# Kernel tuning notes

Hardware: AMD Instinct MI355X
Metric: run time of the kernel (lower is better)

The kernel has to match this reference:

```python
import jax, jax.numpy as jnp
import numpy as np

VOCAB = 32000
EMB = 256
HID = 512
BATCH = 32
MAXLEN = 64
START_TOKEN = 0


def setup_inputs() -> dict:
    key = jax.random.key(0)
    ks = jax.random.split(key, 10)
    return {
        "encoder_outputs": jax.random.normal(ks[0], (BATCH, 64, HID), dtype=jnp.float32),
        "encoder_hidden": jax.random.normal(ks[1], (1, BATCH, HID), dtype=jnp.float32),
        "target_tensor": jax.random.randint(ks[2], (BATCH, MAXLEN), 0, VOCAB),
        "embedding": jax.random.normal(ks[3], (VOCAB, EMB), dtype=jnp.float32) * 0.02,
        "W_ih": jax.random.normal(ks[4], (3 * HID, EMB), dtype=jnp.float32) * 0.05,
        "W_hh": jax.random.normal(ks[5], (3 * HID, HID), dtype=jnp.float32) * 0.05,
        "b_ih": jax.random.normal(ks[6], (3 * HID,), dtype=jnp.float32) * 0.05,
        "b_hh": jax.random.normal(ks[7], (3 * HID,), dtype=jnp.float32) * 0.05,
        "W_out": jax.random.normal(ks[8], (VOCAB, HID), dtype=jnp.float32) * 0.05,
        "b_out": jax.random.normal(ks[9], (VOCAB,), dtype=jnp.float32) * 0.05,
    }


def _gru_scan(x_seq, h0, W_ih, W_hh, b_ih, b_hh):
    # x_seq: [T, B, E]; h0: [B, H]. torch nn.GRU gate math/order (r, z, n).
    def step(h, x):
        gi = x @ W_ih.T + b_ih            # [B, 3H]
        gh = h @ W_hh.T + b_hh            # [B, 3H]
        i_r, i_z, i_n = jnp.split(gi, 3, axis=-1)
        h_r, h_z, h_n = jnp.split(gh, 3, axis=-1)
        r = jax.nn.sigmoid(i_r + h_r)
        z = jax.nn.sigmoid(i_z + h_z)
        n = jnp.tanh(i_n + r * h_n)
        h_new = (1.0 - z) * n + z * h
        return h_new, h_new
    hT, ys = jax.lax.scan(step, h0, x_seq)
    return ys, hT


def reference(encoder_outputs, encoder_hidden, target_tensor, embedding,
              W_ih, W_hh, b_ih, b_hh, W_out, b_out):
    B = encoder_outputs.shape[0]
    # Teacher forcing: step 0 consumes START, step i consumes target[:, i-1].
    start = jnp.full((B, 1), START_TOKEN, dtype=target_tensor.dtype)
    dec_in = jnp.concatenate([start, target_tensor[:, :-1]], axis=1)  # [B, T]
    # embed -> (dropout p=0 is identity) -> relu
    emb = jax.nn.relu(embedding[dec_in])                # [B, T, E]
    x_seq = jnp.swapaxes(emb, 0, 1)                     # [T, B, E]
    h0 = encoder_hidden[0]                              # [B, H] (num_layers=1)
    ys, hT = _gru_scan(x_seq, h0, W_ih, W_hh, b_ih, b_hh)  # ys: [T, B, H]
    hidden_seq = jnp.swapaxes(ys, 0, 1)                 # [B, T, H]
    logits = jnp.einsum("bth,vh->btv", hidden_seq, W_out) + b_out  # [B, T, V]
    log_probs = jax.nn.log_softmax(logits, axis=-1)
    decoder_hidden = hT[None]                           # [1, B, H]
    return log_probs, decoder_hidden
```

## Files before the change

kernel.cpp:

```cpp
#include <hip/hip_runtime.h>
#include <hip/hip_bf16.h>
#include <math.h>


typedef __bf16 bf16x8 __attribute__((ext_vector_type(8)));
typedef float  f32x4  __attribute__((ext_vector_type(4)));
typedef unsigned short u16;
typedef u16 u16x8v __attribute__((ext_vector_type(8)));
typedef u16 u16x4v __attribute__((ext_vector_type(4)));

#define BTV (32L * 64 * 32000)
#define LDC2 64000L

#define OFF_X    (0L)
#define SZ_X     (2048L * 256 * 2)
#define OFF_WIH  (OFF_X + SZ_X)
#define SZ_WIH   (1536L * 256 * 2)
#define OFF_WHH  (OFF_WIH + SZ_WIH)
#define SZ_WHH   (1536L * 512 * 2)
#define OFF_WOUT (OFF_WHH + SZ_WHH)
#define SZ_WOUT  (32000L * 512 * 2)
#define OFF_GI   (OFF_WOUT + SZ_WOUT)
#define SZ_GI    (2048L * 1536 * 4)
#define OFF_HS   (OFF_GI + SZ_GI)
#define SZ_HS    (2048L * 512 * 2)
#define OFF_FLG  (OFF_HS + SZ_HS)
#define SZ_FLG   (512L)
#define OFF_EV   (OFF_FLG + SZ_FLG)
#define SZ_EV    (64L)
#define WS_NEED  (OFF_EV + SZ_EV)

__device__ __forceinline__ u16 f2bf(float f) {
  union { float f; unsigned u; } a; a.f = f;
  unsigned r = a.u + 0x7fffu + ((a.u >> 16) & 1u);
  return (u16)(r >> 16);
}

__device__ __forceinline__ float bf2f(u16 u) {
  union { unsigned u; float f; } a; a.u = ((unsigned)u) << 16;
  return a.f;
}

__device__ __forceinline__ void gload16(const void* g, void* l) {
  __builtin_amdgcn_global_load_lds(
      (const __attribute__((address_space(1))) unsigned int*)g,
      (__attribute__((address_space(3))) unsigned int*)l, 16, 0, 0);
}

extern "C" __global__ void k_cast(const float* __restrict__ s, u16* __restrict__ d, int n4) {
  int i = blockIdx.x * blockDim.x + threadIdx.x;
  int st = gridDim.x * blockDim.x;
  for (; i < n4; i += st) {
    float4 v = reinterpret_cast<const float4*>(s)[i];
    u16x4v o; o.x = f2bf(v.x); o.y = f2bf(v.y); o.z = f2bf(v.z); o.w = f2bf(v.w);
    reinterpret_cast<u16x4v*>(d)[i] = o;
  }
}

extern "C" __global__ void k_embed(const float* __restrict__ emb, const int* __restrict__ tgt,
                                   u16* __restrict__ X) {
  int idx = blockIdx.x * 256 + threadIdx.x;
  int row = idx >> 5;
  int c8  = (idx & 31) << 3;
  int t = row >> 5, b = row & 31;
  int token = (t == 0) ? 0 : tgt[b * 64 + t - 1];
  const float* e = emb + (long)token * 256 + c8;
  u16x8v o;
#pragma unroll
  for (int i = 0; i < 8; ++i) { float v = e[i]; o[i] = f2bf(v > 0.f ? v : 0.f); }
  *reinterpret_cast<u16x8v*>(X + (long)row * 256 + c8) = o;
}

extern "C" __global__ void k_init(unsigned* flags, unsigned* evars) {
  int i = threadIdx.x;
  if (i < 128) {
    unsigned z = 0u;
    asm volatile("global_store_dword %0, %1, off sc0 sc1"
                 :: "v"(flags + i), "v"(z) : "memory");
  }
  if (i < 10) atomicExch(&evars[i], i == 8 ? 0xFFFFFFFFu : 0u);
}

template <bool BF16OUT>
__global__ void __launch_bounds__(256)
k_gemm_t(const u16* __restrict__ A, const u16* __restrict__ B,
         const float* __restrict__ bias, float* __restrict__ C,
         u16* __restrict__ C2, int M, int N, int K, long ldc2) {
  __shared__ u16 At[128 * 32];
  __shared__ u16 Bt[128 * 32];
  int mt = M >> 7;
  int bn = blockIdx.x / mt, bm = blockIdx.x % mt;
  int tid = threadIdx.x, wave = tid >> 6, lane = tid & 63;
  int wr = wave >> 1, wc = wave & 1;
  f32x4 acc[4][4] = {};
  const u16* ga = A + (long)(bm * 128 + wave * 32 + (lane >> 2)) * K + ((lane & 3) << 3);
  const u16* gb = B + (long)(bn * 128 + wave * 32 + (lane >> 2)) * K + ((lane & 3) << 3);
  u16* la0 = &At[wave * 1024]; u16* la1 = la0 + 512;
  u16* lb0 = &Bt[wave * 1024]; u16* lb1 = lb0 + 512;
  long k16 = 16L * K;
  for (int k0 = 0; k0 < K; k0 += 32) {
    if (k0) __syncthreads();
    gload16(ga + k0, la0);
    gload16(ga + k16 + k0, la1);
    gload16(gb + k0, lb0);
    gload16(gb + k16 + k0, lb1);
    __syncthreads();
    bf16x8 af[4], bfr[4];
#pragma unroll
    for (int mi = 0; mi < 4; ++mi)
      af[mi] = *reinterpret_cast<const bf16x8*>(
          &At[(wr * 64 + mi * 16 + (lane & 15)) * 32 + ((lane >> 4) << 3)]);
#pragma unroll
    for (int ni = 0; ni < 4; ++ni)
      bfr[ni] = *reinterpret_cast<const bf16x8*>(
          &Bt[(wc * 64 + ni * 16 + (lane & 15)) * 32 + ((lane >> 4) << 3)]);
#pragma unroll
    for (int mi = 0; mi < 4; ++mi)
#pragma unroll
      for (int ni = 0; ni < 4; ++ni)
        acc[mi][ni] = __builtin_amdgcn_mfma_f32_16x16x32_bf16(af[mi], bfr[ni], acc[mi][ni], 0, 0, 0);
  }
  int rb = bm * 128 + wr * 64 + ((lane >> 4) << 2);
  int cb = bn * 128 + wc * 64 + (lane & 15);
#pragma unroll
  for (int mi = 0; mi < 4; ++mi)
#pragma unroll
    for (int ni = 0; ni < 4; ++ni) {
      int col = cb + ni * 16;
      float bv = bias[col];
#pragma unroll
      for (int q = 0; q < 4; ++q) {
        int rr = rb + mi * 16 + q;
        if (BF16OUT) C2[(long)rr * ldc2 + col] = f2bf(acc[mi][ni][q] + bv);
        else         C[(long)rr * N + col] = acc[mi][ni][q] + bv;
      }
    }
}

extern "C" __global__ void __launch_bounds__(768, 1)
k_gru6(const float* __restrict__ gi, const u16* __restrict__ Whh,
       const float* __restrict__ bhh, const float* __restrict__ eh,
       u16* __restrict__ HS, float* __restrict__ outH,
       unsigned* flags, unsigned* evars) {
  __shared__ u16 Ah[32 * 512];
  __shared__ float gh[3][2][32][66];
  __shared__ int role_s;
  int tid = threadIdx.x, wave = tid >> 6, lane = tid & 63;
  if (tid == 0) {
    unsigned xcc;
    asm volatile("s_getreg_b32 %0, hwreg(20, 0, 32)" : "=s"(xcc));
    xcc &= 7u;
    unsigned arr = atomicAdd(&evars[xcc], 1u);
    if (arr == 7u) atomicCAS(&evars[8], 0xFFFFFFFFu, xcc);
    unsigned L = 0xFFFFFFFFu;
    for (int it = 0; it < (1 << 24) && L == 0xFFFFFFFFu; ++it) {
      asm volatile("global_load_dword %0, %1, off sc0 sc1\n\ts_waitcnt vmcnt(0)"
                   : "=v"(L) : "v"(evars + 8) : "memory");
    }
    int role = -1;
    if (L == xcc) {
      unsigned c = atomicAdd(&evars[9], 1u);
      if (c < 8u) role = (int)c;
    }
    role_s = role;
  }
  __syncthreads();
  int g = role_s;
  if (g < 0) return;
  int j0 = g * 64;
  int gate = wave >> 2, uh = (wave >> 1) & 1, sig = wave & 1;
  bf16x8 barr[2][8];
  {
    const u16* wbase = Whh + (long)(gate * 512 + j0 + uh * 32) * 512 + sig * 256;
#pragma unroll
    for (int ut = 0; ut < 2; ++ut)
#pragma unroll
      for (int kt = 0; kt < 8; ++kt)
        barr[ut][kt] = *reinterpret_cast<const bf16x8*>(
            wbase + (long)(ut * 16 + (lane & 15)) * 512 + kt * 32 + ((lane >> 4) << 3));
  }
  bool act2 = tid < 512;
  float hprev[3] = {}, bb0[3] = {}, bb1[3] = {}, bb2[3] = {};
  const float* gp0; const float* gp1; const float* gp2 = nullptr;
  u16* hs0; u16* hs1; u16* hs2 = nullptr;
  int b_[3], u_[3];
#pragma unroll
  for (int s = 0; s < 3; ++s) {
    int o = s * 768 + tid;
    if (o < 2048) {
      int b = o >> 6, u = o & 63, j = j0 + u;
      b_[s] = b; u_[s] = u;
      hprev[s] = eh[b * 512 + j];
      bb0[s] = bhh[j]; bb1[s] = bhh[512 + j]; bb2[s] = bhh[1024 + j];
    } else { b_[s] = 0; u_[s] = 0; }
  }
  gp0 = gi + b_[0] * 1536 + j0 + u_[0];
  gp1 = gi + b_[1] * 1536 + j0 + u_[1];
  if (act2) gp2 = gi + b_[2] * 1536 + j0 + u_[2];
  hs0 = HS + ((long)b_[0] * 64) * 512 + j0 + u_[0];
  hs1 = HS + ((long)b_[1] * 64) * 512 + j0 + u_[1];
  if (act2) hs2 = HS + ((long)b_[2] * 64) * 512 + j0 + u_[2];
  const char* sp0 = nullptr; const char* sp1 = nullptr;
  const char* sp2 = nullptr; const char* sp3 = nullptr;
  char* ld0 = nullptr; char* ld1 = nullptr; char* ld2 = nullptr; char* ld3 = nullptr;
  if (tid < 512) {
#pragma unroll
    for (int l = 0; l < 4; ++l) {
      int n = l * 512 + tid;
      int row = n >> 6, i = n & 63;
      const char* sp = (const char*)HS + (long)row * 65536 + i * 16 - 1024;
      char* ld = (char*)Ah + row * 1024 + ((i * 16) ^ ((row & 7) << 4));
      if (l == 0) { sp0 = sp; ld0 = ld; } else if (l == 1) { sp1 = sp; ld1 = ld; }
      else if (l == 2) { sp2 = sp; ld2 = ld; } else { sp3 = sp; ld3 = ld; }
    }
#pragma unroll
    for (int l = 0; l < 4; ++l) {
      int n = l * 512 + tid;
      int row = n >> 6, i = n & 63;
      const float* p = eh + row * 512 + i * 8;
      float4 aa = *reinterpret_cast<const float4*>(p);
      float4 bb = *reinterpret_cast<const float4*>(p + 4);
      u16x8v o8;
      o8[0] = f2bf(aa.x); o8[1] = f2bf(aa.y); o8[2] = f2bf(aa.z); o8[3] = f2bf(aa.w);
      o8[4] = f2bf(bb.x); o8[5] = f2bf(bb.y); o8[6] = f2bf(bb.z); o8[7] = f2bf(bb.w);
      *reinterpret_cast<u16x8v*>((char*)Ah + row * 1024 + ((i * 16) ^ ((row & 7) << 4))) = o8;
    }
  }
  const float K1 = -1.44269504f, K2 = 2.88539009f;
  for (int t = 0; t < 64; ++t) {
    float gr0 = gp0[0], gz0 = gp0[512], gn0 = gp0[1024];
    float gr1 = gp1[0], gz1 = gp1[512], gn1 = gp1[1024];
    float gr2 = 0.f, gz2 = 0.f, gn2 = 0.f;
    if (act2) { gr2 = gp2[0]; gz2 = gp2[512]; gn2 = gp2[1024]; }
    gp0 += 49152; gp1 += 49152; if (act2) gp2 += 49152;
    if (t) {
      if (wave == 0) {
        const unsigned* fp = flags + (lane & 7) * 16;
        unsigned v;
        do {
          asm volatile("global_load_dword %0, %1, off sc0 sc1\n\ts_waitcnt vmcnt(0)"
                       : "=v"(v) : "v"(fp) : "memory");
        } while (!__all((int)(v >= (unsigned)t)));
      }
      __syncthreads();
      if (tid < 512) {
        f32x4 d0, d1, d2, d3;
        asm volatile(
            "global_load_dwordx4 %0, %4, off sc0\n\t"
            "global_load_dwordx4 %1, %5, off sc0\n\t"
            "global_load_dwordx4 %2, %6, off sc0\n\t"
            "global_load_dwordx4 %3, %7, off sc0\n\t"
            "s_waitcnt vmcnt(0)"
            : "=v"(d0), "=v"(d1), "=v"(d2), "=v"(d3)
            : "v"(sp0), "v"(sp1), "v"(sp2), "v"(sp3)
            : "memory");
        *reinterpret_cast<f32x4*>(ld0) = d0;
        *reinterpret_cast<f32x4*>(ld1) = d1;
        *reinterpret_cast<f32x4*>(ld2) = d2;
        *reinterpret_cast<f32x4*>(ld3) = d3;
      }
    }
    if (tid < 512) { sp0 += 1024; sp1 += 1024; sp2 += 1024; sp3 += 1024; }
    __syncthreads();
    f32x4 acc[2][2] = {};
    int r15 = lane & 15;
    int cbyte = sig * 512 + ((lane >> 4) << 4);
#pragma unroll
    for (int kt = 0; kt < 8; ++kt) {
      bf16x8 a0 = *reinterpret_cast<const bf16x8*>(
          (const char*)Ah + r15 * 1024 + ((kt * 64 + cbyte) ^ ((r15 & 7) << 4)));
      bf16x8 a1 = *reinterpret_cast<const bf16x8*>(
          (const char*)Ah + (16 + r15) * 1024 + ((kt * 64 + cbyte) ^ ((r15 & 7) << 4)));
#pragma unroll
      for (int ut = 0; ut < 2; ++ut) {
        acc[0][ut] = __builtin_amdgcn_mfma_f32_16x16x32_bf16(a0, barr[ut][kt], acc[0][ut], 0, 0, 0);
        acc[1][ut] = __builtin_amdgcn_mfma_f32_16x16x32_bf16(a1, barr[ut][kt], acc[1][ut], 0, 0, 0);
      }
    }
    {
      int ucol = uh * 32 + r15;
      int brow = (lane >> 4) << 2;
#pragma unroll
      for (int q = 0; q < 4; ++q) {
        gh[gate][sig][brow + q][ucol]           = acc[0][0][q];
        gh[gate][sig][brow + q][ucol + 16]      = acc[0][1][q];
        gh[gate][sig][16 + brow + q][ucol]      = acc[1][0][q];
        gh[gate][sig][16 + brow + q][ucol + 16] = acc[1][1][q];
      }
    }
    __syncthreads();
#pragma unroll
    for (int s = 0; s < 3; ++s) {
      if (s == 2 && !act2) break;
      int b = b_[s], u = u_[s];
      float gr = s == 0 ? gr0 : s == 1 ? gr1 : gr2;
      float gz = s == 0 ? gz0 : s == 1 ? gz1 : gz2;
      float gn = s == 0 ? gn0 : s == 1 ? gn1 : gn2;
      float hr = gh[0][0][b][u] + gh[0][1][b][u] + bb0[s];
      float hz = gh[1][0][b][u] + gh[1][1][b][u] + bb1[s];
      float hn = gh[2][0][b][u] + gh[2][1][b][u] + bb2[s];
      float r = 1.f / (1.f + __builtin_amdgcn_exp2f(K1 * (gr + hr)));
      float z = 1.f / (1.f + __builtin_amdgcn_exp2f(K1 * (gz + hz)));
      float x = gn + r * hn;
      float th = 1.f - 2.f / (1.f + __builtin_amdgcn_exp2f(K2 * x));
      float hnew = th + z * (hprev[s] - th);
      hprev[s] = hnew;
      unsigned hb = (unsigned)f2bf(hnew);
      u16* hp = s == 0 ? hs0 : s == 1 ? hs1 : hs2;
      asm volatile("global_store_short %0, %1, off sc0"
                   :: "v"(hp), "v"(hb) : "memory");
    }
    hs0 += 512; hs1 += 512; if (act2) hs2 += 512;
    asm volatile("s_waitcnt vmcnt(0)" ::: "memory");
    __syncthreads();
    if (tid == 0) {
      unsigned ph = (unsigned)(t + 1);
      asm volatile("global_store_dword %0, %1, off sc0 sc1\n\ts_waitcnt vmcnt(0)"
                   :: "v"(flags + g * 16), "v"(ph) : "memory");
    }
  }
#pragma unroll
  for (int s = 0; s < 3; ++s) {
    if (s == 2 && !act2) break;
    outH[b_[s] * 512 + j0 + u_[s]] = hprev[s];
  }
}

extern "C" __global__ void __launch_bounds__(512)
k_lsm_b(const u16* __restrict__ LGbase, float* __restrict__ P) {
  extern __shared__ u16 srb[];
  __shared__ float red[8];
  const u16* LG = LGbase + (long)blockIdx.x * LDC2;
  float* out = P + (long)blockIdx.x * 32000;
  int tid = threadIdx.x, wave = tid >> 6, lane = tid & 63;
  float mx = -INFINITY;
  for (int i = tid; i < 4000; i += 512) {
    u16x8v v = reinterpret_cast<const u16x8v*>(LG)[i];
    reinterpret_cast<u16x8v*>(srb)[i] = v;
#pragma unroll
    for (int e = 0; e < 8; ++e) mx = fmaxf(mx, bf2f(v[e]));
  }
#pragma unroll
  for (int off = 32; off; off >>= 1) mx = fmaxf(mx, __shfl_down(mx, off, 64));
  if (lane == 0) red[wave] = mx;
  __syncthreads();
  if (tid == 0) {
    float m = red[0];
#pragma unroll
    for (int w = 1; w < 8; ++w) m = fmaxf(m, red[w]);
    red[0] = m;
  }
  __syncthreads();
  mx = red[0];
  __syncthreads();
  float sm = 0.f;
  for (int i = tid; i < 4000; i += 512) {
    u16x8v v = reinterpret_cast<const u16x8v*>(srb)[i];
#pragma unroll
    for (int e = 0; e < 8; ++e) sm += __expf(bf2f(v[e]) - mx);
  }
#pragma unroll
  for (int off = 32; off; off >>= 1) sm += __shfl_down(sm, off, 64);
  if (lane == 0) red[wave] = sm;
  __syncthreads();
  if (tid == 0) {
    float s = 0.f;
#pragma unroll
    for (int w = 0; w < 8; ++w) s += red[w];
    red[0] = mx + __logf(s);
  }
  __syncthreads();
  float L = red[0];
  for (int i = tid; i < 4000; i += 512) {
    u16x8v v = reinterpret_cast<const u16x8v*>(srb)[i];
    float4 o1, o2;
    o1.x = bf2f(v[0]) - L; o1.y = bf2f(v[1]) - L; o1.z = bf2f(v[2]) - L; o1.w = bf2f(v[3]) - L;
    o2.x = bf2f(v[4]) - L; o2.y = bf2f(v[5]) - L; o2.z = bf2f(v[6]) - L; o2.w = bf2f(v[7]) - L;
    reinterpret_cast<float4*>(out + (long)i * 8)[0] = o1;
    reinterpret_cast<float4*>(out + (long)i * 8)[1] = o2;
  }
}

extern "C" void kernel_launch(void* const* d_in, const int* in_sizes, int n_in,
                              void* d_out, int out_size, void* d_ws, size_t ws_size,
                              hipStream_t stream) {
  (void)in_sizes; (void)n_in; (void)out_size;
  const float* enc_hid = (const float*)d_in[1];
  const int*   tgt     = (const int*)d_in[2];
  const float* emb     = (const float*)d_in[3];
  const float* W_ih    = (const float*)d_in[4];
  const float* W_hh    = (const float*)d_in[5];
  const float* b_ih    = (const float*)d_in[6];
  const float* b_hh    = (const float*)d_in[7];
  const float* W_out   = (const float*)d_in[8];
  const float* b_out   = (const float*)d_in[9];
  float* out = (float*)d_out;
  char* ws = (char*)d_ws;
  if (ws_size < (size_t)WS_NEED) return;

  u16* X        = (u16*)(ws + OFF_X);
  u16* Wih      = (u16*)(ws + OFF_WIH);
  u16* Whh      = (u16*)(ws + OFF_WHH);
  u16* Wout     = (u16*)(ws + OFF_WOUT);
  float* gi     = (float*)(ws + OFF_GI);
  u16* HS       = (u16*)(ws + OFF_HS);
  unsigned* flg = (unsigned*)(ws + OFF_FLG);
  unsigned* ev  = (unsigned*)(ws + OFF_EV);
  u16* LG       = (u16*)d_out;

  hipFuncSetAttribute(reinterpret_cast<const void*>(k_lsm_b),
                      hipFuncAttributeMaxDynamicSharedMemorySize, 65536);

  k_cast<<<96, 256, 0, stream>>>(W_ih, Wih, 1536 * 256 / 4);
  k_cast<<<192, 256, 0, stream>>>(W_hh, Whh, 1536 * 512 / 4);
  k_cast<<<2048, 256, 0, stream>>>(W_out, Wout, 32000 * 512 / 4);
  k_embed<<<256, 256, 0, stream>>>(emb, tgt, X);
  k_init<<<1, 256, 0, stream>>>(flg, ev);
  k_gemm_t<false><<<(1536 / 128) * (2048 / 128), 256, 0, stream>>>(
      X, Wih, b_ih, gi, nullptr, 2048, 1536, 256, 0);
  k_gru6<<<64, 768, 0, stream>>>(gi, Whh, b_hh, enc_hid, HS, out + BTV, flg, ev);
  k_gemm_t<true><<<(32000 / 128) * (2048 / 128), 256, 0, stream>>>(
      HS, Wout, b_out, nullptr, LG, 2048, 32000, 512, LDC2);
  k_lsm_b<<<2048, 512, 64000, stream>>>(LG, out);
}
```

Measured before the change: 450.3 us.

## Fuse GRU recurrence and output projection into one persistent megakernel

The GRU recurrence and the vocabulary projection GEMM are merged into a single persistent kernel. Eight blocks run the GRU, and the remaining blocks poll per-step flags to start projection tiles for time steps whose hidden states are complete, so the large GEMM overlaps the serial recurrence. HS is re-laid out time-major so that each row tile corresponds to finished time steps, with output rows remapped back. Both GEMMs gain double-buffered LDS prefetch. The risks are spin-wait overhead, three blocks sharing a CU with the latency-critical GRU blocks, and possible deadlock if the co-residency assumptions do not hold.

Measured after the change: 734.9 us. 63.2% more time.

```diff
diff --git a/kernel.cpp b/kernel.cpp
--- a/kernel.cpp
+++ b/kernel.cpp
@@ -11,6 +11,8 @@
 
 #define BTV (32L * 64 * 32000)
 #define LDC2 64000L
+#define NPROJ 248
+#define NTILES 4000
 
 #define OFF_X    (0L)
 #define SZ_X     (2048L * 256 * 2)
@@ -25,7 +27,7 @@
 #define OFF_HS   (OFF_GI + SZ_GI)
 #define SZ_HS    (2048L * 512 * 2)
 #define OFF_FLG  (OFF_HS + SZ_HS)
-#define SZ_FLG   (512L)
+#define SZ_FLG   (1024L)
 #define OFF_EV   (OFF_FLG + SZ_FLG)
 #define SZ_EV    (64L)
 #define WS_NEED  (OFF_EV + SZ_EV)
@@ -73,21 +75,20 @@
 
 extern "C" __global__ void k_init(unsigned* flags, unsigned* evars) {
   int i = threadIdx.x;
-  if (i < 128) {
+  if (i < 256) {
     unsigned z = 0u;
     asm volatile("global_store_dword %0, %1, off sc0 sc1"
                  :: "v"(flags + i), "v"(z) : "memory");
   }
-  if (i < 10) atomicExch(&evars[i], i == 8 ? 0xFFFFFFFFu : 0u);
-}
-
-template <bool BF16OUT>
-__global__ void __launch_bounds__(256)
-k_gemm_t(const u16* __restrict__ A, const u16* __restrict__ B,
-         const float* __restrict__ bias, float* __restrict__ C,
-         u16* __restrict__ C2, int M, int N, int K, long ldc2) {
-  __shared__ u16 At[128 * 32];
-  __shared__ u16 Bt[128 * 32];
+  if (i < 12) atomicExch(&evars[i], i == 8 ? 0xFFFFFFFFu : 0u);
+}
+
+extern "C" __global__ void __launch_bounds__(256)
+k_gemm_gi(const u16* __restrict__ A, const u16* __restrict__ B,
+          const float* __restrict__ bias, float* __restrict__ C,
+          int M, int N, int K) {
+  __shared__ u16 At[2][4096];
+  __shared__ u16 Bt[2][4096];
   int mt = M >> 7;
   int bn = blockIdx.x / mt, bm = blockIdx.x % mt;
   int tid = threadIdx.x, wave = tid >> 6, lane = tid & 63;
@@ -95,30 +96,39 @@
   f32x4 acc[4][4] = {};
   const u16* ga = A + (long)(bm * 128 + wave * 32 + (lane >> 2)) * K + ((lane & 3) << 3);
   const u16* gb = B + (long)(bn * 128 + wave * 32 + (lane >> 2)) * K + ((lane & 3) << 3);
-  u16* la0 = &At[wave * 1024]; u16* la1 = la0 + 512;
-  u16* lb0 = &Bt[wave * 1024]; u16* lb1 = lb0 + 512;
   long k16 = 16L * K;
+  {
+    u16* la0 = &At[0][wave * 1024]; u16* lb0 = &Bt[0][wave * 1024];
+    gload16(ga, la0); gload16(ga + k16, la0 + 512);
+    gload16(gb, lb0); gload16(gb + k16, lb0 + 512);
+  }
+  asm volatile("s_waitcnt vmcnt(0)" ::: "memory");
+  __syncthreads();
+  int cur = 0;
   for (int k0 = 0; k0 < K; k0 += 32) {
-    if (k0) __syncthreads();
-    gload16(ga + k0, la0);
-    gload16(ga + k16 + k0, la1);
-    gload16(gb + k0, lb0);
-    gload16(gb + k16 + k0, lb1);
-    __syncthreads();
+    if (k0 + 32 < K) {
+      int nb = cur ^ 1;
+      u16* la0 = &At[nb][wave * 1024]; u16* lb0 = &Bt[nb][wave * 1024];
+      gload16(ga + k0 + 32, la0); gload16(ga + k16 + k0 + 32, la0 + 512);
+      gload16(gb + k0 + 32, lb0); gload16(gb + k16 + k0 + 32, lb0 + 512);
+    }
     bf16x8 af[4], bfr[4];
 #pragma unroll
     for (int mi = 0; mi < 4; ++mi)
       af[mi] = *reinterpret_cast<const bf16x8*>(
-          &At[(wr * 64 + mi * 16 + (lane & 15)) * 32 + ((lane >> 4) << 3)]);
+          &At[cur][(wr * 64 + mi * 16 + (lane & 15)) * 32 + ((lane >> 4) << 3)]);
 #pragma unroll
     for (int ni = 0; ni < 4; ++ni)
       bfr[ni] = *reinterpret_cast<const bf16x8*>(
-          &Bt[(wc * 64 + ni * 16 + (lane & 15)) * 32 + ((lane >> 4) << 3)]);
+          &Bt[cur][(wc * 64 + ni * 16 + (lane & 15)) * 32 + ((lane >> 4) << 3)]);
 #pragma unroll
     for (int mi = 0; mi < 4; ++mi)
 #pragma unroll
       for (int ni = 0; ni < 4; ++ni)
         acc[mi][ni] = __builtin_amdgcn_mfma_f32_16x16x32_bf16(af[mi], bfr[ni], acc[mi][ni], 0, 0, 0);
+    asm volatile("s_waitcnt vmcnt(0)" ::: "memory");
+    __syncthreads();
+    cur ^= 1;
   }
   int rb = bm * 128 + wr * 64 + ((lane >> 4) << 2);
   int cb = bn * 128 + wc * 64 + (lane & 15);
@@ -131,20 +141,21 @@
 #pragma unroll
       for (int q = 0; q < 4; ++q) {
         int rr = rb + mi * 16 + q;
-        if (BF16OUT) C2[(long)rr * ldc2 + col] = f2bf(acc[mi][ni][q] + bv);
-        else         C[(long)rr * N + col] = acc[mi][ni][q] + bv;
-      }
-    }
-}
-
-extern "C" __global__ void __launch_bounds__(768, 1)
-k_gru6(const float* __restrict__ gi, const u16* __restrict__ Whh,
+        C[(long)rr * N + col] = acc[mi][ni][q] + bv;
+      }
+    }
+}
+
+extern "C" __global__ void __launch_bounds__(768, 3)
+k_mega(const float* __restrict__ gi, const u16* __restrict__ Whh,
        const float* __restrict__ bhh, const float* __restrict__ eh,
        u16* __restrict__ HS, float* __restrict__ outH,
-       unsigned* flags, unsigned* evars) {
-  __shared__ u16 Ah[32 * 512];
-  __shared__ float gh[3][2][32][66];
+       unsigned* flags, unsigned* evars,
+       const u16* __restrict__ Wout, const float* __restrict__ bout,
+       u16* __restrict__ LG) {
+  extern __shared__ char arena[];
   __shared__ int role_s;
+  __shared__ int pidx_s;
   int tid = threadIdx.x, wave = tid >> 6, lane = tid & 63;
   if (tid == 0) {
     unsigned xcc;
@@ -166,163 +177,251 @@
   }
   __syncthreads();
   int g = role_s;
-  if (g < 0) return;
-  int j0 = g * 64;
-  int gate = wave >> 2, uh = (wave >> 1) & 1, sig = wave & 1;
-  bf16x8 barr[2][8];
-  {
-    const u16* wbase = Whh + (long)(gate * 512 + j0 + uh * 32) * 512 + sig * 256;
-#pragma unroll
-    for (int ut = 0; ut < 2; ++ut)
-#pragma unroll
-      for (int kt = 0; kt < 8; ++kt)
-        barr[ut][kt] = *reinterpret_cast<const bf16x8*>(
-            wbase + (long)(ut * 16 + (lane & 15)) * 512 + kt * 32 + ((lane >> 4) << 3));
-  }
-  bool act2 = tid < 512;
-  float hprev[3] = {}, bb0[3] = {}, bb1[3] = {}, bb2[3] = {};
-  const float* gp0; const float* gp1; const float* gp2 = nullptr;
-  u16* hs0; u16* hs1; u16* hs2 = nullptr;
-  int b_[3], u_[3];
-#pragma unroll
-  for (int s = 0; s < 3; ++s) {
-    int o = s * 768 + tid;
-    if (o < 2048) {
-      int b = o >> 6, u = o & 63, j = j0 + u;
-      b_[s] = b; u_[s] = u;
-      hprev[s] = eh[b * 512 + j];
-      bb0[s] = bhh[j]; bb1[s] = bhh[512 + j]; bb2[s] = bhh[1024 + j];
-    } else { b_[s] = 0; u_[s] = 0; }
-  }
-  gp0 = gi + b_[0] * 1536 + j0 + u_[0];
-  gp1 = gi + b_[1] * 1536 + j0 + u_[1];
-  if (act2) gp2 = gi + b_[2] * 1536 + j0 + u_[2];
-  hs0 = HS + ((long)b_[0] * 64) * 512 + j0 + u_[0];
-  hs1 = HS + ((long)b_[1] * 64) * 512 + j0 + u_[1];
-  if (act2) hs2 = HS + ((long)b_[2] * 64) * 512 + j0 + u_[2];
-  const char* sp0 = nullptr; const char* sp1 = nullptr;
-  const char* sp2 = nullptr; const char* sp3 = nullptr;
-  char* ld0 = nullptr; char* ld1 = nullptr; char* ld2 = nullptr; char* ld3 = nullptr;
-  if (tid < 512) {
-#pragma unroll
-    for (int l = 0; l < 4; ++l) {
-      int n = l * 512 + tid;
-      int row = n >> 6, i = n & 63;
-      const char* sp = (const char*)HS + (long)row * 65536 + i * 16 - 1024;
-      char* ld = (char*)Ah + row * 1024 + ((i * 16) ^ ((row & 7) << 4));
-      if (l == 0) { sp0 = sp; ld0 = ld; } else if (l == 1) { sp1 = sp; ld1 = ld; }
-      else if (l == 2) { sp2 = sp; ld2 = ld; } else { sp3 = sp; ld3 = ld; }
-    }
-#pragma unroll
-    for (int l = 0; l < 4; ++l) {
-      int n = l * 512 + tid;
-      int row = n >> 6, i = n & 63;
-      const float* p = eh + row * 512 + i * 8;
-      float4 aa = *reinterpret_cast<const float4*>(p);
-      float4 bb = *reinterpret_cast<const float4*>(p + 4);
-      u16x8v o8;
-      o8[0] = f2bf(aa.x); o8[1] = f2bf(aa.y); o8[2] = f2bf(aa.z); o8[3] = f2bf(aa.w);
-      o8[4] = f2bf(bb.x); o8[5] = f2bf(bb.y); o8[6] = f2bf(bb.z); o8[7] = f2bf(bb.w);
-      *reinterpret_cast<u16x8v*>((char*)Ah + row * 1024 + ((i * 16) ^ ((row & 7) << 4))) = o8;
-    }
-  }
-  const float K1 = -1.44269504f, K2 = 2.88539009f;
-  for (int t = 0; t < 64; ++t) {
-    float gr0 = gp0[0], gz0 = gp0[512], gn0 = gp0[1024];
-    float gr1 = gp1[0], gz1 = gp1[512], gn1 = gp1[1024];
-    float gr2 = 0.f, gz2 = 0.f, gn2 = 0.f;
-    if (act2) { gr2 = gp2[0]; gz2 = gp2[512]; gn2 = gp2[1024]; }
-    gp0 += 49152; gp1 += 49152; if (act2) gp2 += 49152;
-    if (t) {
-      if (wave == 0) {
-        const unsigned* fp = flags + (lane & 7) * 16;
-        unsigned v;
-        do {
-          asm volatile("global_load_dword %0, %1, off sc0 sc1\n\ts_waitcnt vmcnt(0)"
-                       : "=v"(v) : "v"(fp) : "memory");
-        } while (!__all((int)(v >= (unsigned)t)));
-      }
-      __syncthreads();
-      if (tid < 512) {
-        f32x4 d0, d1, d2, d3;
-        asm volatile(
-            "global_load_dwordx4 %0, %4, off sc0\n\t"
-            "global_load_dwordx4 %1, %5, off sc0\n\t"
-            "global_load_dwordx4 %2, %6, off sc0\n\t"
-            "global_load_dwordx4 %3, %7, off sc0\n\t"
-            "s_waitcnt vmcnt(0)"
-            : "=v"(d0), "=v"(d1), "=v"(d2), "=v"(d3)
-            : "v"(sp0), "v"(sp1), "v"(sp2), "v"(sp3)
-            : "memory");
-        *reinterpret_cast<f32x4*>(ld0) = d0;
-        *reinterpret_cast<f32x4*>(ld1) = d1;
-        *reinterpret_cast<f32x4*>(ld2) = d2;
-        *reinterpret_cast<f32x4*>(ld3) = d3;
-      }
-    }
-    if (tid < 512) { sp0 += 1024; sp1 += 1024; sp2 += 1024; sp3 += 1024; }
-    __syncthreads();
-    f32x4 acc[2][2] = {};
+
+  if (g >= 0) {
+    u16* Ah = (u16*)arena;
+    float (*gh)[2][32][66] = (float (*)[2][32][66])(arena + 32768);
+    int j0 = g * 64;
+    int gate = wave >> 2, uh = (wave >> 1) & 1, sig = wave & 1;
+    bf16x8 barr[2][8];
+    {
+      const u16* wbase = Whh + (long)(gate * 512 + j0 + uh * 32) * 512 + sig * 256;
+#pragma unroll
+      for (int ut = 0; ut < 2; ++ut)
+#pragma unroll
+        for (int kt = 0; kt < 8; ++kt)
+          barr[ut][kt] = *reinterpret_cast<const bf16x8*>(
+              wbase + (long)(ut * 16 + (lane & 15)) * 512 + kt * 32 + ((lane >> 4) << 3));
+    }
+    bool act2 = tid < 512;
+    float hprev[3] = {}, bb0[3] = {}, bb1[3] = {}, bb2[3] = {};
+    int b_[3], u_[3];
+#pragma unroll
+    for (int s = 0; s < 3; ++s) {
+      int o = s * 768 + tid;
+      if (o < 2048) {
+        int b = o >> 6, u = o & 63, j = j0 + u;
+        b_[s] = b; u_[s] = u;
+        hprev[s] = eh[b * 512 + j];
+        bb0[s] = bhh[j]; bb1[s] = bhh[512 + j]; bb2[s] = bhh[1024 + j];
+      } else { b_[s] = 0; u_[s] = 0; }
+    }
+    const float* gp0 = gi + (long)b_[0] * 1536 + j0 + u_[0];
+    const float* gp1 = gi + (long)b_[1] * 1536 + j0 + u_[1];
+    const float* gp2 = act2 ? gi + (long)b_[2] * 1536 + j0 + u_[2] : nullptr;
+    u16* hs0 = HS + (long)b_[0] * 512 + j0 + u_[0];
+    u16* hs1 = HS + (long)b_[1] * 512 + j0 + u_[1];
+    u16* hs2 = act2 ? HS + (long)b_[2] * 512 + j0 + u_[2] : nullptr;
+    const char* sp0 = nullptr; const char* sp1 = nullptr;
+    const char* sp2 = nullptr; const char* sp3 = nullptr;
+    char* ld0 = nullptr; char* ld1 = nullptr; char* ld2 = nullptr; char* ld3 = nullptr;
+    if (tid < 512) {
+#pragma unroll
+      for (int l = 0; l < 4; ++l) {
+        int n = l * 512 + tid;
+        int row = n >> 6, i = n & 63;
+        char* ld = (char*)Ah + row * 1024 + ((i * 16) ^ ((row & 7) << 4));
+        const char* sp = (const char*)HS + (long)n * 16 - 32768;
+        if (l == 0) { sp0 = sp; ld0 = ld; } else if (l == 1) { sp1 = sp; ld1 = ld; }
+        else if (l == 2) { sp2 = sp; ld2 = ld; } else { sp3 = sp; ld3 = ld; }
+      }
+#pragma unroll
+      for (int l = 0; l < 4; ++l) {
+        int n = l * 512 + tid;
+        int row = n >> 6, i = n & 63;
+        const float* p = eh + row * 512 + i * 8;
+        float4 aa = *reinterpret_cast<const float4*>(p);
+        float4 bb = *reinterpret_cast<const float4*>(p + 4);
+        u16x8v o8;
+        o8[0] = f2bf(aa.x); o8[1] = f2bf(aa.y); o8[2] = f2bf(aa.z); o8[3] = f2bf(aa.w);
+        o8[4] = f2bf(bb.x); o8[5] = f2bf(bb.y); o8[6] = f2bf(bb.z); o8[7] = f2bf(bb.w);
+        *reinterpret_cast<u16x8v*>((char*)Ah + row * 1024 + ((i * 16) ^ ((row & 7) << 4))) = o8;
+      }
+    }
     int r15 = lane & 15;
     int cbyte = sig * 512 + ((lane >> 4) << 4);
-#pragma unroll
-    for (int kt = 0; kt < 8; ++kt) {
-      bf16x8 a0 = *reinterpret_cast<const bf16x8*>(
-          (const char*)Ah + r15 * 1024 + ((kt * 64 + cbyte) ^ ((r15 & 7) << 4)));
-      bf16x8 a1 = *reinterpret_cast<const bf16x8*>(
-          (const char*)Ah + (16 + r15) * 1024 + ((kt * 64 + cbyte) ^ ((r15 & 7) << 4)));
-#pragma unroll
-      for (int ut = 0; ut < 2; ++ut) {
-        acc[0][ut] = __builtin_amdgcn_mfma_f32_16x16x32_bf16(a0, barr[ut][kt], acc[0][ut], 0, 0, 0);
-        acc[1][ut] = __builtin_amdgcn_mfma_f32_16x16x32_bf16(a1, barr[ut][kt], acc[1][ut], 0, 0, 0);
-      }
-    }
-    {
-      int ucol = uh * 32 + r15;
-      int brow = (lane >> 4) << 2;
-#pragma unroll
-      for (int q = 0; q < 4; ++q) {
-        gh[gate][sig][brow + q][ucol]           = acc[0][0][q];
-        gh[gate][sig][brow + q][ucol + 16]      = acc[0][1][q];
-        gh[gate][sig][16 + brow + q][ucol]      = acc[1][0][q];
-        gh[gate][sig][16 + brow + q][ucol + 16] = acc[1][1][q];
-      }
-    }
-    __syncthreads();
+    int ucol = uh * 32 + r15;
+    int brow = (lane >> 4) << 2;
+    const float K1 = -1.44269504f, K2 = 2.88539009f;
+    for (int t = 0; t < 64; ++t) {
+      float gr0 = gp0[0], gz0 = gp0[512], gn0 = gp0[1024]; gp0 += 49152;
+      float gr1 = gp1[0], gz1 = gp1[512], gn1 = gp1[1024]; gp1 += 49152;
+      float gr2 = 0.f, gz2 = 0.f, gn2 = 0.f;
+      if (act2) { gr2 = gp2[0]; gz2 = gp2[512]; gn2 = gp2[1024]; gp2 += 49152; }
+      if (t) {
+        if (wave == 0) {
+          const unsigned* fp = flags + (lane & 7) * 16;
+          unsigned v;
+          do {
+            asm volatile("global_load_dword %0, %1, off sc0 sc1\n\ts_waitcnt vmcnt(0)"
+                         : "=v"(v) : "v"(fp) : "memory");
+          } while (!__all((int)(v >= (unsigned)t)));
+        }
+        __syncthreads();
+        if (tid < 512) {
+          f32x4 d0, d1, d2, d3;
+          asm volatile(
+              "global_load_dwordx4 %0, %4, off sc0\n\t"
+              "global_load_dwordx4 %1, %5, off sc0\n\t"
+              "global_load_dwordx4 %2, %6, off sc0\n\t"
+              "global_load_dwordx4 %3, %7, off sc0\n\t"
+              "s_waitcnt vmcnt(0)"
+              : "=v"(d0), "=v"(d1), "=v"(d2), "=v"(d3)
+              : "v"(sp0), "v"(sp1), "v"(sp2), "v"(sp3)
+              : "memory");
+          *reinterpret_cast<f32x4*>(ld0) = d0;
+          *reinterpret_cast<f32x4*>(ld1) = d1;
+          *reinterpret_cast<f32x4*>(ld2) = d2;
+          *reinterpret_cast<f32x4*>(ld3) = d3;
+        }
+      }
+      if (tid < 512) { sp0 += 32768; sp1 += 32768; sp2 += 32768; sp3 += 32768; }
+      __syncthreads();
+      {
+        f32x4 acc[2][2] = {};
+#pragma unroll
+        for (int kt = 0; kt < 8; ++kt) {
+          bf16x8 a0 = *reinterpret_cast<const bf16x8*>(
+              (const char*)Ah + r15 * 1024 + ((kt * 64 + cbyte) ^ ((r15 & 7) << 4)));
+          bf16x8 a1 = *reinterpret_cast<const bf16x8*>(
+              (const char*)Ah + (16 + r15) * 1024 + ((kt * 64 + cbyte) ^ ((r15 & 7) << 4)));
+#pragma unroll
+          for (int ut = 0; ut < 2; ++ut) {
+            acc[0][ut] = __builtin_amdgcn_mfma_f32_16x16x32_bf16(a0, barr[ut][kt], acc[0][ut], 0, 0, 0);
+            acc[1][ut] = __builtin_amdgcn_mfma_f32_16x16x32_bf16(a1, barr[ut][kt], acc[1][ut], 0, 0, 0);
+          }
+        }
+#pragma unroll
+        for (int q = 0; q < 4; ++q) {
+          gh[gate][sig][brow + q][ucol]           = acc[0][0][q];
+          gh[gate][sig][brow + q][ucol + 16]      = acc[0][1][q];
+          gh[gate][sig][16 + brow + q][ucol]      = acc[1][0][q];
+          gh[gate][sig][16 + brow + q][ucol + 16] = acc[1][1][q];
+        }
+      }
+      __syncthreads();
+#pragma unroll
+      for (int s = 0; s < 3; ++s) {
+        if (s == 2 && !act2) break;
+        int b = b_[s], u = u_[s];
+        float gr = s == 0 ? gr0 : s == 1 ? gr1 : gr2;
+        float gz = s == 0 ? gz0 : s == 1 ? gz1 : gz2;
+        float gn = s == 0 ? gn0 : s == 1 ? gn1 : gn2;
+        float hr = gh[0][0][b][u] + gh[0][1][b][u] + bb0[s];
+        float hz = gh[1][0][b][u] + gh[1][1][b][u] + bb1[s];
+        float hn = gh[2][0][b][u] + gh[2][1][b][u] + bb2[s];
+        float r = 1.f / (1.f + __builtin_amdgcn_exp2f(K1 * (gr + hr)));
+        float z = 1.f / (1.f + __builtin_amdgcn_exp2f(K1 * (gz + hz)));
+        float x = gn + r * hn;
+        float th = 1.f - 2.f / (1.f + __builtin_amdgcn_exp2f(K2 * x));
+        float hnew = th + z * (hprev[s] - th);
+        hprev[s] = hnew;
+        unsigned hb = (unsigned)f2bf(hnew);
+        u16* hp = s == 0 ? hs0 : s == 1 ? hs1 : hs2;
+        asm volatile("global_store_short %0, %1, off sc0 sc1"
+                     :: "v"(hp), "v"(hb) : "memory");
+      }
+      hs0 += 16384; hs1 += 16384; if (act2) hs2 += 16384;
+      asm volatile("s_waitcnt vmcnt(0)" ::: "memory");
+      __syncthreads();
+      if (tid == 704) {
+        unsigned ph = (unsigned)(t + 1);
+        asm volatile("global_store_dword %0, %1, off sc0 sc1\n\ts_waitcnt vmcnt(0)"
+                     :: "v"(flags + g * 16), "v"(ph) : "memory");
+      }
+    }
 #pragma unroll
     for (int s = 0; s < 3; ++s) {
       if (s == 2 && !act2) break;
-      int b = b_[s], u = u_[s];
-      float gr = s == 0 ? gr0 : s == 1 ? gr1 : gr2;
-      float gz = s == 0 ? gz0 : s == 1 ? gz1 : gz2;
-      float gn = s == 0 ? gn0 : s == 1 ? gn1 : gn2;
-      float hr = gh[0][0][b][u] + gh[0][1][b][u] + bb0[s];
-      float hz = gh[1][0][b][u] + gh[1][1][b][u] + bb1[s];
-      float hn = gh[2][0][b][u] + gh[2][1][b][u] + bb2[s];
-      float r = 1.f / (1.f + __builtin_amdgcn_exp2f(K1 * (gr + hr)));
-      float z = 1.f / (1.f + __builtin_amdgcn_exp2f(K1 * (gz + hz)));
-      float x = gn + r * hn;
-      float th = 1.f - 2.f / (1.f + __builtin_amdgcn_exp2f(K2 * x));
-      float hnew = th + z * (hprev[s] - th);
-      hprev[s] = hnew;
-      unsigned hb = (unsigned)f2bf(hnew);
-      u16* hp = s == 0 ? hs0 : s == 1 ? hs1 : hs2;
-      asm volatile("global_store_short %0, %1, off sc0"
-                   :: "v"(hp), "v"(hb) : "memory");
-    }
-    hs0 += 512; hs1 += 512; if (act2) hs2 += 512;
+      outH[b_[s] * 512 + j0 + u_[s]] = hprev[s];
+    }
+    return;
+  }
+
+  if (tid == 0) pidx_s = (int)atomicAdd(&evars[10], 1u);
+  __syncthreads();
+  int p = pidx_s;
+  int grp = wave >> 2, wv = wave & 3;
+  int wr = wv >> 1, wc = wv & 1;
+  u16* At = (u16*)(arena + grp * 32768);
+  u16* Bt = At + 8192;
+  const long k16 = 16L * 512;
+  for (long round = 0;; ++round) {
+    long base = 3L * p + 3L * NPROJ * round;
+    if (base >= NTILES) break;
+    int lastTile = (int)((base + 2 < NTILES) ? base + 2 : (NTILES - 1));
+    unsigned need = 4u * (unsigned)(lastTile / 250) + 4u;
+    if (wave == 0) {
+      const unsigned* fp = flags + (lane & 7) * 16;
+      unsigned v; int it = 0;
+      for (;;) {
+        asm volatile("global_load_dword %0, %1, off sc0 sc1\n\ts_waitcnt vmcnt(0)"
+                     : "=v"(v) : "v"(fp) : "memory");
+        if (__all((int)(v >= need)) || ++it > (1 << 22)) break;
+        asm volatile("s_sleep 16");
+      }
+    }
+    __syncthreads();
+    int myTile = (int)base + grp;
+    bool active = myTile < NTILES;
+    int mt = active ? myTile / 250 : 0;
+    int nt = active ? myTile % 250 : 0;
+    f32x4 acc[4][4] = {};
+    const u16* ga = HS + (long)(mt * 128 + wv * 32 + (lane >> 2)) * 512 + ((lane & 3) << 3);
+    const u16* gb = Wout + (long)(nt * 128 + wv * 32 + (lane >> 2)) * 512 + ((lane & 3) << 3);
+    if (active) {
+      gload16(ga, &At[wv * 1024]);        gload16(ga + k16, &At[wv * 1024 + 512]);
+      gload16(gb, &Bt[wv * 1024]);        gload16(gb + k16, &Bt[wv * 1024 + 512]);
+    }
     asm volatile("s_waitcnt vmcnt(0)" ::: "memory");
     __syncthreads();
-    if (tid == 0) {
-      unsigned ph = (unsigned)(t + 1);
-      asm volatile("global_store_dword %0, %1, off sc0 sc1\n\ts_waitcnt vmcnt(0)"
-                   :: "v"(flags + g * 16), "v"(ph) : "memory");
-    }
-  }
-#pragma unroll
-  for (int s = 0; s < 3; ++s) {
-    if (s == 2 && !act2) break;
-    outH[b_[s] * 512 + j0 + u_[s]] = hprev[s];
+    int cur = 0;
+    for (int k0 = 0; k0 < 512; k0 += 32) {
+      if (active && k0 + 32 < 512) {
+        int nb = cur ^ 1;
+        gload16(ga + k0 + 32, &At[nb * 4096 + wv * 1024]);
+        gload16(ga + k16 + k0 + 32, &At[nb * 4096 + wv * 1024 + 512]);
+        gload16(gb + k0 + 32, &Bt[nb * 4096 + wv * 1024]);
+        gload16(gb + k16 + k0 + 32, &Bt[nb * 4096 + wv * 1024 + 512]);
+      }
+      if (active) {
+        bf16x8 af[4], bfr[4];
+#pragma unroll
+        for (int mi = 0; mi < 4; ++mi)
+          af[mi] = *reinterpret_cast<const bf16x8*>(
+              &At[cur * 4096 + (wr * 64 + mi * 16 + (lane & 15)) * 32 + ((lane >> 4) << 3)]);
+#pragma unroll
+        for (int ni = 0; ni < 4; ++ni)
+          bfr[ni] = *reinterpret_cast<const bf16x8*>(
+              &Bt[cur * 4096 + (wc * 64 + ni * 16 + (lane & 15)) * 32 + ((lane >> 4) << 3)]);
+#pragma unroll
+        for (int mi = 0; mi < 4; ++mi)
+#pragma unroll
+          for (int ni = 0; ni < 4; ++ni)
+            acc[mi][ni] = __builtin_amdgcn_mfma_f32_16x16x32_bf16(af[mi], bfr[ni], acc[mi][ni], 0, 0, 0);
+      }
+      asm volatile("s_waitcnt vmcnt(0)" ::: "memory");
+      __syncthreads();
+      cur ^= 1;
+    }
+    if (active) {
+      int rb = mt * 128 + wr * 64 + ((lane >> 4) << 2);
+      int cb = nt * 128 + wc * 64 + (lane & 15);
+#pragma unroll
+      for (int mi = 0; mi < 4; ++mi)
+#pragma unroll
+        for (int ni = 0; ni < 4; ++ni) {
+          int col = cb + ni * 16;
+          float bv = bout[col];
+#pragma unroll
+          for (int q = 0; q < 4; ++q) {
+            int r = rb + mi * 16 + q;
+            long orow = (long)(r & 31) * 64 + (r >> 5);
+            LG[orow * LDC2 + col] = f2bf(acc[mi][ni][q] + bv);
+          }
+        }
+    }
+    __syncthreads();
   }
 }
 
@@ -408,6 +507,8 @@
   unsigned* ev  = (unsigned*)(ws + OFF_EV);
   u16* LG       = (u16*)d_out;
 
+  hipFuncSetAttribute(reinterpret_cast<const void*>(k_mega),
+                      hipFuncAttributeMaxDynamicSharedMemorySize, 98304);
   hipFuncSetAttribute(reinterpret_cast<const void*>(k_lsm_b),
                       hipFuncAttributeMaxDynamicSharedMemorySize, 65536);
 
@@ -416,10 +517,9 @@
   k_cast<<<2048, 256, 0, stream>>>(W_out, Wout, 32000 * 512 / 4);
   k_embed<<<256, 256, 0, stream>>>(emb, tgt, X);
   k_init<<<1, 256, 0, stream>>>(flg, ev);
-  k_gemm_t<false><<<(1536 / 128) * (2048 / 128), 256, 0, stream>>>(
-      X, Wih, b_ih, gi, nullptr, 2048, 1536, 256, 0);
-  k_gru6<<<64, 768, 0, stream>>>(gi, Whh, b_hh, enc_hid, HS, out + BTV, flg, ev);
-  k_gemm_t<true><<<(32000 / 128) * (2048 / 128), 256, 0, stream>>>(
-      HS, Wout, b_out, nullptr, LG, 2048, 32000, 512, LDC2);
+  k_gemm_gi<<<(1536 / 128) * (2048 / 128), 256, 0, stream>>>(
+      X, Wih, b_ih, gi, 2048, 1536, 256);
+  k_mega<<<256, 768, 98304, stream>>>(gi, Whh, b_hh, enc_hid, HS, out + BTV,
+                                      flg, ev, Wout, b_out, LG);
   k_lsm_b<<<2048, 512, 64000, stream>>>(LG, out);
 }
```

## Overlap W_out cast with GRU scan and double-buffer GEMM tiles

Applied to the files above, without the earlier changes.

The standalone W_out fp32-to-bf16 cast kernel is removed. The 56 GRU blocks that lose the role election now do that cast while the 8 elected blocks run the serial recurrence, so the cast hides behind the latency-bound scan. The GEMM gains LDS double buffering, prefetching the next K-slice while MFMAs run on the current one, and a block-index swizzle that spreads tiles across XCDs. Extra flag and evar slots are initialised for the work-distribution ticket counter. The cost is extra memory traffic that competes with the GRU blocks and doubled GEMM shared memory.

Result: faster. 429.8 us, median of 2 (-4.5%).

```diff
diff --git a/kernel.cpp b/kernel.cpp
--- a/kernel.cpp
+++ b/kernel.cpp
@@ -25,7 +25,7 @@
 #define OFF_HS   (OFF_GI + SZ_GI)
 #define SZ_HS    (2048L * 512 * 2)
 #define OFF_FLG  (OFF_HS + SZ_HS)
-#define SZ_FLG   (512L)
+#define SZ_FLG   (1024L)
 #define OFF_EV   (OFF_FLG + SZ_FLG)
 #define SZ_EV    (64L)
 #define WS_NEED  (OFF_EV + SZ_EV)
@@ -73,12 +73,12 @@
 
 extern "C" __global__ void k_init(unsigned* flags, unsigned* evars) {
   int i = threadIdx.x;
-  if (i < 128) {
+  if (i < 256) {
     unsigned z = 0u;
     asm volatile("global_store_dword %0, %1, off sc0 sc1"
                  :: "v"(flags + i), "v"(z) : "memory");
   }
-  if (i < 10) atomicExch(&evars[i], i == 8 ? 0xFFFFFFFFu : 0u);
+  if (i < 12) atomicExch(&evars[i], i == 8 ? 0xFFFFFFFFu : 0u);
 }
 
 template <bool BF16OUT>
@@ -86,39 +86,50 @@
 k_gemm_t(const u16* __restrict__ A, const u16* __restrict__ B,
          const float* __restrict__ bias, float* __restrict__ C,
          u16* __restrict__ C2, int M, int N, int K, long ldc2) {
-  __shared__ u16 At[128 * 32];
-  __shared__ u16 Bt[128 * 32];
+  __shared__ u16 At[2][4096];
+  __shared__ u16 Bt[2][4096];
   int mt = M >> 7;
-  int bn = blockIdx.x / mt, bm = blockIdx.x % mt;
+  int i = blockIdx.x;
+  int j = (i & 7) * ((int)gridDim.x >> 3) + (i >> 3);
+  int bn = j / mt, bm = j % mt;
   int tid = threadIdx.x, wave = tid >> 6, lane = tid & 63;
   int wr = wave >> 1, wc = wave & 1;
   f32x4 acc[4][4] = {};
   const u16* ga = A + (long)(bm * 128 + wave * 32 + (lane >> 2)) * K + ((lane & 3) << 3);
   const u16* gb = B + (long)(bn * 128 + wave * 32 + (lane >> 2)) * K + ((lane & 3) << 3);
-  u16* la0 = &At[wave * 1024]; u16* la1 = la0 + 512;
-  u16* lb0 = &Bt[wave * 1024]; u16* lb1 = lb0 + 512;
   long k16 = 16L * K;
+  {
+    u16* la0 = &At[0][wave * 1024]; u16* lb0 = &Bt[0][wave * 1024];
+    gload16(ga, la0); gload16(ga + k16, la0 + 512);
+    gload16(gb, lb0); gload16(gb + k16, lb0 + 512);
+  }
+  asm volatile("s_waitcnt vmcnt(0)" ::: "memory");
+  __syncthreads();
+  int cur = 0;
   for (int k0 = 0; k0 < K; k0 += 32) {
-    if (k0) __syncthreads();
-    gload16(ga + k0, la0);
-    gload16(ga + k16 + k0, la1);
-    gload16(gb + k0, lb0);
-    gload16(gb + k16 + k0, lb1);
-    __syncthreads();
+    if (k0 + 32 < K) {
+      int nb = cur ^ 1;
+      u16* la0 = &At[nb][wave * 1024]; u16* lb0 = &Bt[nb][wave * 1024];
+      gload16(ga + k0 + 32, la0); gload16(ga + k16 + k0 + 32, la0 + 512);
+      gload16(gb + k0 + 32, lb0); gload16(gb + k16 + k0 + 32, lb0 + 512);
+    }
     bf16x8 af[4], bfr[4];
 #pragma unroll
     for (int mi = 0; mi < 4; ++mi)
       af[mi] = *reinterpret_cast<const bf16x8*>(
-          &At[(wr * 64 + mi * 16 + (lane & 15)) * 32 + ((lane >> 4) << 3)]);
+          &At[cur][(wr * 64 + mi * 16 + (lane & 15)) * 32 + ((lane >> 4) << 3)]);
 #pragma unroll
     for (int ni = 0; ni < 4; ++ni)
       bfr[ni] = *reinterpret_cast<const bf16x8*>(
-          &Bt[(wc * 64 + ni * 16 + (lane & 15)) * 32 + ((lane >> 4) << 3)]);
+          &Bt[cur][(wc * 64 + ni * 16 + (lane & 15)) * 32 + ((lane >> 4) << 3)]);
 #pragma unroll
     for (int mi = 0; mi < 4; ++mi)
 #pragma unroll
       for (int ni = 0; ni < 4; ++ni)
         acc[mi][ni] = __builtin_amdgcn_mfma_f32_16x16x32_bf16(af[mi], bfr[ni], acc[mi][ni], 0, 0, 0);
+    asm volatile("s_waitcnt vmcnt(0)" ::: "memory");
+    __syncthreads();
+    cur ^= 1;
   }
   int rb = bm * 128 + wr * 64 + ((lane >> 4) << 2);
   int cb = bn * 128 + wc * 64 + (lane & 15);
@@ -138,13 +149,15 @@
 }
 
 extern "C" __global__ void __launch_bounds__(768, 1)
-k_gru6(const float* __restrict__ gi, const u16* __restrict__ Whh,
+k_gru9(const float* __restrict__ gi, const u16* __restrict__ Whh,
        const float* __restrict__ bhh, const float* __restrict__ eh,
        u16* __restrict__ HS, float* __restrict__ outH,
-       unsigned* flags, unsigned* evars) {
+       unsigned* flags, unsigned* evars,
+       const float* __restrict__ Wof, u16* __restrict__ WoutB) {
   __shared__ u16 Ah[32 * 512];
   __shared__ float gh[3][2][32][66];
   __shared__ int role_s;
+  __shared__ int tick_s;
   int tid = threadIdx.x, wave = tid >> 6, lane = tid & 63;
   if (tid == 0) {
     unsigned xcc;
@@ -166,7 +179,19 @@
   }
   __syncthreads();
   int g = role_s;
-  if (g < 0) return;
+  if (g < 0) {
+    if (tid == 0) tick_s = (int)atomicAdd(&evars[11], 1u);
+    __syncthreads();
+    long c = (long)tick_s;
+    const float4* src = reinterpret_cast<const float4*>(Wof);
+    u16x4v* dst = reinterpret_cast<u16x4v*>(WoutB);
+    for (long idx = c * 768 + tid; idx < 4096000L; idx += 56L * 768) {
+      float4 v = src[idx];
+      u16x4v o; o.x = f2bf(v.x); o.y = f2bf(v.y); o.z = f2bf(v.z); o.w = f2bf(v.w);
+      dst[idx] = o;
+    }
+    return;
+  }
   int j0 = g * 64;
   int gate = wave >> 2, uh = (wave >> 1) & 1, sig = wave & 1;
   bf16x8 barr[2][8];
@@ -194,9 +219,9 @@
       bb0[s] = bhh[j]; bb1[s] = bhh[512 + j]; bb2[s] = bhh[1024 + j];
     } else { b_[s] = 0; u_[s] = 0; }
   }
-  gp0 = gi + b_[0] * 1536 + j0 + u_[0];
-  gp1 = gi + b_[1] * 1536 + j0 + u_[1];
-  if (act2) gp2 = gi + b_[2] * 1536 + j0 + u_[2];
+  gp0 = gi + (long)b_[0] * 1536 + j0 + u_[0];
+  gp1 = gi + (long)b_[1] * 1536 + j0 + u_[1];
+  if (act2) gp2 = gi + (long)b_[2] * 1536 + j0 + u_[2];
   hs0 = HS + ((long)b_[0] * 64) * 512 + j0 + u_[0];
   hs1 = HS + ((long)b_[1] * 64) * 512 + j0 + u_[1];
   if (act2) hs2 = HS + ((long)b_[2] * 64) * 512 + j0 + u_[2];
@@ -413,12 +438,12 @@
 
   k_cast<<<96, 256, 0, stream>>>(W_ih, Wih, 1536 * 256 / 4);
   k_cast<<<192, 256, 0, stream>>>(W_hh, Whh, 1536 * 512 / 4);
-  k_cast<<<2048, 256, 0, stream>>>(W_out, Wout, 32000 * 512 / 4);
   k_embed<<<256, 256, 0, stream>>>(emb, tgt, X);
   k_init<<<1, 256, 0, stream>>>(flg, ev);
   k_gemm_t<false><<<(1536 / 128) * (2048 / 128), 256, 0, stream>>>(
       X, Wih, b_ih, gi, nullptr, 2048, 1536, 256, 0);
-  k_gru6<<<64, 768, 0, stream>>>(gi, Whh, b_hh, enc_hid, HS, out + BTV, flg, ev);
+  k_gru9<<<64, 768, 0, stream>>>(gi, Whh, b_hh, enc_hid, HS, out + BTV, flg, ev,
+                                 W_out, Wout);
   k_gemm_t<true><<<(32000 / 128) * (2048 / 128), 256, 0, stream>>>(
       HS, Wout, b_out, nullptr, LG, 2048, 32000, 512, LDC2);
   k_lsm_b<<<2048, 512, 64000, stream>>>(LG, out);
```
